# Kernel tuning notes

Hardware: AMD Instinct MI355X
Metric: run time of the kernel (lower is better)

Reference implementation:

```python
import jax, jax.numpy as jnp
import numpy as np

BLOCK = (4, 8, 8)   # (t, h, w)
NH, D, DA = 8, 512, 64
EPS = 1e-5


def _layernorm(x, g, b):
    m = jnp.mean(x, axis=-1, keepdims=True)
    xc = x - m
    v = jnp.mean(xc * xc, axis=-1, keepdims=True)
    return xc * jax.lax.rsqrt(v + EPS) * g + b


def setup_inputs() -> dict:
    key = jax.random.key(0)
    ks = jax.random.split(key, 10)
    B, T, H, W = 2, 8, 32, 32
    t, h, w = BLOCK
    s_qkv = (2.0 / (D + DA)) ** 0.5   # xavier_normal for (d, da) fan
    s_lin = (2.0 / (D + D)) ** 0.5
    return {
        "x": jax.random.normal(ks[0], (B, D, T, H, W), jnp.float32),
        "dt_bank": 0.02 * jax.random.normal(ks[1], (NH, 2 * t - 1), jnp.float32),
        "dh_bank": 0.02 * jax.random.normal(ks[2], (NH, 2 * h - 1), jnp.float32),
        "dw_bank": 0.02 * jax.random.normal(ks[3], (NH, 2 * w - 1), jnp.float32),
        "ln1_g": jnp.ones((D,), jnp.float32),
        "ln1_b": jnp.zeros((D,), jnp.float32),
        "w_q": s_qkv * jax.random.normal(ks[4], (NH, D, DA), jnp.float32),
        "w_k": s_qkv * jax.random.normal(ks[5], (NH, D, DA), jnp.float32),
        "w_v": s_qkv * jax.random.normal(ks[6], (NH, D, DA), jnp.float32),
        "w_proj": s_lin * jax.random.normal(ks[7], (D, NH * DA), jnp.float32),
        "ln2_g": jnp.ones((D,), jnp.float32),
        "ln2_b": jnp.zeros((D,), jnp.float32),
        "w1": s_lin * jax.random.normal(ks[8], (D, D), jnp.float32),
        "b1": jnp.zeros((D,), jnp.float32),
        "w2": s_lin * jax.random.normal(ks[9], (D, D), jnp.float32),
        "b2": jnp.zeros((D,), jnp.float32),
    }


def _axial_bias(dt_bank, dh_bank, dw_bank):
    t, h, w = BLOCK
    thw = t * h * w
    ar = jnp.arange(thw)
    tt = ar // (h * w)
    hh = (ar // w) % h
    ww = ar % w
    # relative offsets shifted to be non-negative (matches dt += abs(dt.min()))
    it = tt[:, None] - tt[None, :] + (t - 1)
    ih = hh[:, None] - hh[None, :] + (h - 1)
    iw = ww[:, None] - ww[None, :] + (w - 1)
    return dt_bank[:, it] + dh_bank[:, ih] + dw_bank[:, iw]  # (NH, thw, thw)


def reference(x, dt_bank, dh_bank, dw_bank, ln1_g, ln1_b, w_q, w_k, w_v,
              w_proj, ln2_g, ln2_b, w1, b1, w2, b2):
    B, C, T, H, W = x.shape
    t, h, w = BLOCK
    st, sh, sw = T // t, H // h, W // w
    thw = t * h * w
    nb = B * st * sh * sw

    # block split: (B,C,T,H,W) -> (nb, thw, C)
    xb = x.reshape(B, C, st, t, sh, h, sw, w).transpose(0, 2, 4, 6, 1, 3, 5, 7)
    xb = xb.reshape(nb, C, thw).transpose(0, 2, 1)

    Bb = _axial_bias(dt_bank, dh_bank, dw_bank)  # (NH, thw, thw)

    # --- multi-head attention with additive axial bias ---
    resid = xb
    xn = _layernorm(xb, ln1_g, ln1_b)
    q = jnp.einsum('bnd,hde->hbne', xn, w_q)
    k = jnp.einsum('bnd,hde->hbne', xn, w_k)
    v = jnp.einsum('bnd,hde->hbne', xn, w_v)
    scale = 1.0 / jnp.sqrt(jnp.asarray(DA, x.dtype))
    attn = jnp.einsum('hbne,hbme->hbnm', q, k) * scale + Bb[:, None]
    attn = jax.nn.softmax(attn, axis=-1)
    out = jnp.einsum('hbnm,hbme->hbne', attn, v)         # (NH, nb, thw, DA)
    out = out.transpose(1, 2, 0, 3).reshape(nb, thw, NH * DA)  # head-major concat
    out = out @ w_proj.T + resid

    # --- FFN with residual ---
    y = _layernorm(out, ln2_g, ln2_b)
    y = jax.nn.relu(y @ w1.T + b1) @ w2.T + b2
    out = y + out

    # un-block: (nb, thw, C) -> (B,C,T,H,W)
    out = out.transpose(0, 2, 1).reshape(B, st, sh, sw, C, t, h, w)
    out = out.transpose(0, 4, 1, 5, 2, 6, 3, 7).reshape(B, C, T, H, W)
    return out
```

## Files before the change

### kernel.cpp

```cpp
#include <hip/hip_runtime.h>
#include <hip/hip_bf16.h>
#include <stdint.h>

typedef __attribute__((ext_vector_type(4))) float f32x4;
typedef __attribute__((ext_vector_type(8))) short s16x8;
typedef __attribute__((ext_vector_type(4))) short s16x4;
typedef __attribute__((ext_vector_type(8))) __bf16 b16x8;

__device__ __forceinline__ f32x4 mfma16(s16x8 a, s16x8 b, f32x4 c) {
  return __builtin_amdgcn_mfma_f32_16x16x32_bf16(
      __builtin_bit_cast(b16x8, a), __builtin_bit_cast(b16x8, b), c, 0, 0, 0);
}

__device__ __forceinline__ void gl_lds16(const void* g, void* l) {
  __builtin_amdgcn_global_load_lds(
      (const __attribute__((address_space(1))) void*)g,
      (__attribute__((address_space(3))) void*)l, 16, 0, 0);
}

__device__ __forceinline__ unsigned short f2bf(float f) {
  union { float f; unsigned u; } v; v.f = f;
  unsigned u = v.u;
  return (unsigned short)((u + 0x7FFFu + ((u >> 16) & 1u)) >> 16);
}

__device__ __forceinline__ float bf2f(unsigned short u) {
  union { unsigned u; float f; } v; v.u = ((unsigned)u) << 16; return v.f;
}

__device__ __forceinline__ unsigned cvt_pk_bf16(float a, float b) {
  unsigned r;
  asm("v_cvt_pk_bf16_f32 %0, %1, %2" : "=v"(r) : "v"(a), "v"(b));
  return r;
}

#if __has_builtin(__builtin_amdgcn_exp2f)
#define EXP2F(x) __builtin_amdgcn_exp2f(x)
#else
#define EXP2F(x) exp2f(x)
#endif

__device__ __forceinline__ int bfrag_off(int n, int k) {
  return ((((n >> 4) * 16 + (k >> 5)) * 4 + ((k >> 3) & 3)) * 16 + (n & 15)) * 8 + (k & 7);
}

__global__ __launch_bounds__(256) void k_gather_ln(
    const float* __restrict__ x, const float* __restrict__ g1, const float* __restrict__ b1,
    unsigned short* __restrict__ xb, unsigned short* __restrict__ xn,
    const float* __restrict__ wq, const float* __restrict__ wk, const float* __restrict__ wv,
    const float* __restrict__ wp, const float* __restrict__ w1, const float* __restrict__ w2,
    unsigned short* __restrict__ qkvT, unsigned short* __restrict__ wpT,
    unsigned short* __restrict__ w1T, unsigned short* __restrict__ w2T)
{
  if (blockIdx.x >= 1024) {
    int i = (blockIdx.x - 1024) * 256 + threadIdx.x;
    if (i < 786432) {
      int n = i >> 9, d = i & 511;
      const float* src = (n < 512) ? wq : (n < 1024 ? wk : wv);
      int nn = n & 511;
      int h = nn >> 6, e = nn & 63;
      qkvT[bfrag_off(n, d)] = f2bf(src[((size_t)h * 512 + d) * 64 + e]);
    } else {
      int j = i - 786432;
      int w = j >> 18;
      int o = j & 262143;
      const float* s = (w == 0) ? wp : (w == 1 ? w1 : w2);
      unsigned short* dst = (w == 0) ? wpT : (w == 1 ? w1T : w2T);
      dst[bfrag_off(o >> 9, o & 511)] = f2bf(s[o]);
    }
    return;
  }
  __shared__ float lx[16][517];
  int gid = blockIdx.x;
  int h2 = gid & 1, hh = (gid >> 1) & 7, tt = (gid >> 4) & 3,
      shI = (gid >> 6) & 3, stI = (gid >> 8) & 1, bI = (gid >> 9) & 1;
  const float* xbase = x + (size_t)bI * 4194304 + (size_t)(stI * 4 + tt) * 1024
                       + (shI * 8 + hh) * 32 + h2 * 16;
  int t = threadIdx.x;
  for (int i = 0; i < 8; ++i) {
    int slot = i * 256 + t;
    int c = slot >> 2, w8 = slot & 3;
    const float4 v = *(const float4*)(xbase + (size_t)c * 8192 + w8 * 4);
    lx[w8 * 4 + 0][c] = v.x; lx[w8 * 4 + 1][c] = v.y;
    lx[w8 * 4 + 2][c] = v.z; lx[w8 * 4 + 3][c] = v.w;
  }
  __syncthreads();
  int lane = t & 63, wid = t >> 6;
  for (int q = 0; q < 4; ++q) {
    int widx = wid * 4 + q;
    float vv[8]; float s = 0.f, ss = 0.f;
    #pragma unroll
    for (int i = 0; i < 8; ++i) { float v = lx[widx][lane + i * 64]; vv[i] = v; s += v; ss += v * v; }
    #pragma unroll
    for (int d = 1; d < 64; d <<= 1) { s += __shfl_xor(s, d); ss += __shfl_xor(ss, d); }
    float mean = s * (1.f / 512.f);
    float var = ss * (1.f / 512.f) - mean * mean;
    float rs = rsqrtf(var + 1e-5f);
    int sw = h2 * 2 + (widx >> 3), ww = widx & 7;
    int blk = ((bI * 2 + stI) * 4 + shI) * 4 + sw;
    int n = tt * 64 + hh * 8 + ww;
    size_t base = ((size_t)blk * 256 + n) * 512;
    #pragma unroll
    for (int i = 0; i < 8; ++i) {
      int c = lane + i * 64;
      float v = vv[i];
      xb[base + c] = f2bf(v);
      xn[base + c] = f2bf((v - mean) * rs * g1[c] + b1[c]);
    }
  }
}

template<int EPI>
__global__ __launch_bounds__(256, 2) void k_gemm(
    const unsigned short* __restrict__ A, const unsigned short* __restrict__ Bt,
    int M, int N,
    unsigned short* __restrict__ Cbf, float* __restrict__ Cf,
    const float* __restrict__ bias,
    const unsigned short* __restrict__ addbf,
    unsigned short* __restrict__ vTout)
{
  constexpr int K = 512;
  __shared__ __align__(16) unsigned short a_lds[2][128 * 64];
  int tid = threadIdx.x, lane = tid & 63, wid = tid >> 6;
  int lin = blockIdx.y * gridDim.x + blockIdx.x;
  int xcd = lin & 7, idx = lin >> 3;
  int bx = xcd * 16 + (idx & 15);
  int by = idx >> 4;
  int m0 = bx * 128, n0 = by * 128;
  int wm = (wid >> 1) * 64, wn = (wid & 1) * 64;
  int r15 = lane & 15, g = lane >> 4;

  const unsigned short* aptr[4];
  int segoff[4];
  #pragma unroll
  for (int s = 0; s < 4; ++s) {
    int seg = wid * 4 + s;
    int slot = seg * 64 + lane;
    int m = slot >> 3, lc = (slot & 7) ^ (m & 7);
    aptr[s] = A + (size_t)(m0 + m) * K + lc * 8;
    segoff[s] = seg * 1024;
  }
  const unsigned short* bfbase = Bt + (size_t)((n0 + wn) >> 4) * 8192 + lane * 8;

  f32x4 acc[4][4] = {};
  s16x8 b[2][4][2];

  #pragma unroll
  for (int s = 0; s < 4; ++s) gl_lds16(aptr[s], (char*)a_lds[0] + segoff[s]);
  #pragma unroll
  for (int f = 0; f < 4; ++f)
    #pragma unroll
    for (int kk = 0; kk < 2; ++kk)
      b[0][f][kk] = *(const s16x8*)(bfbase + f * 8192 + kk * 512);

  #pragma unroll
  for (int it = 0; it < 8; ++it) {
    int cur = it & 1;
    if (it < 7) {
      int ksn = (it + 1) * 64;
      #pragma unroll
      for (int s = 0; s < 4; ++s)
        gl_lds16(aptr[s] + ksn, (char*)a_lds[cur ^ 1] + segoff[s]);
      asm volatile("s_waitcnt vmcnt(4)" ::: "memory");
    } else {
      asm volatile("s_waitcnt vmcnt(0)" ::: "memory");
    }
    __builtin_amdgcn_s_barrier();
    __builtin_amdgcn_sched_barrier(0);
    if (it < 7) {
      int kc0 = (it + 1) * 2;
      #pragma unroll
      for (int f = 0; f < 4; ++f)
        #pragma unroll
        for (int kk = 0; kk < 2; ++kk)
          b[cur ^ 1][f][kk] = *(const s16x8*)(bfbase + f * 8192 + (kc0 + kk) * 512);
    }
    const char* al = (const char*)a_lds[cur];
    #pragma unroll
    for (int kk = 0; kk < 2; ++kk) {
      s16x8 af[4];
      #pragma unroll
      for (int f = 0; f < 4; ++f) {
        int mm = wm + f * 16 + r15;
        af[f] = *(const s16x8*)(al + mm * 128 + (((kk * 4 + g) ^ (mm & 7)) * 16));
      }
      __builtin_amdgcn_s_setprio(1);
      #pragma unroll
      for (int fm = 0; fm < 4; ++fm)
        #pragma unroll
        for (int fn = 0; fn < 4; ++fn)
          acc[fm][fn] = mfma16(af[fm], b[cur][fn][kk], acc[fm][fn]);
      __builtin_amdgcn_s_setprio(0);
    }
    __builtin_amdgcn_s_barrier();
    __builtin_amdgcn_sched_barrier(0);
  }

  int g4 = g * 4;
  #pragma unroll
  for (int fm = 0; fm < 4; ++fm) {
    #pragma unroll
    for (int fn = 0; fn < 4; ++fn) {
      int col = n0 + wn + fn * 16 + r15;
      int row0 = m0 + wm + fm * 16 + g4;
      if (EPI == 0 && col >= 1024) {
        int h = (col - 1024) >> 6, e = col & 63;
        int blk = row0 >> 8, mtok = row0 & 255;
        s16x4 pk;
        #pragma unroll
        for (int r = 0; r < 4; ++r) pk[r] = (short)f2bf(acc[fm][fn][r]);
        *(s16x4*)(vTout + (((size_t)blk * 8 + h) * 64 + e) * 256 + mtok) = pk;
      } else {
        #pragma unroll
        for (int r = 0; r < 4; ++r) {
          int row = row0 + r;
          float v = acc[fm][fn][r];
          if (EPI == 0) {
            Cbf[(size_t)row * 1536 + col] = f2bf(v);
          } else if (EPI == 1) {
            Cbf[(size_t)row * 512 + col] = f2bf(v + bf2f(addbf[(size_t)row * 512 + col]));
          } else if (EPI == 2) {
            Cbf[(size_t)row * 512 + col] = f2bf(fmaxf(v + bias[col], 0.f));
          } else {
            Cf[(size_t)row * 512 + col] = v + bias[col] + bf2f(addbf[(size_t)row * 512 + col]);
          }
        }
      }
    }
  }
}

__global__ __launch_bounds__(256, 1) void k_attn(
    const unsigned short* __restrict__ qkv, const unsigned short* __restrict__ vT,
    const float* __restrict__ dtb, const float* __restrict__ dhb, const float* __restrict__ dwb,
    unsigned short* __restrict__ aout)
{
  __shared__ __align__(16) unsigned short k_lds[2][64 * 64];
  __shared__ __align__(16) unsigned short v_lds[2][64 * 64];
  __shared__ __align__(16) unsigned short p_lds[4][64 * 64];
  __shared__ float bt_s[8], bh_s[16], bw_s[16];

  const float L2E = 1.44269504f;
  const float SC = 0.125f * 1.44269504f;

  int tid = threadIdx.x, lane = tid & 63, wid = tid >> 6;
  int bk = blockIdx.x >> 3, h = blockIdx.x & 7;
  if (tid < 7) bt_s[tid] = dtb[h * 7 + tid] * L2E;
  else if (tid < 22) bh_s[tid - 7] = dhb[h * 15 + tid - 7] * L2E;
  else if (tid < 37) bw_s[tid - 22] = dwb[h * 15 + tid - 22] * L2E;

  int r15 = lane & 15, g = lane >> 4;
  int wq0 = wid * 64;
  size_t bkBase = (size_t)bk * 256;
  const unsigned short* kbase = qkv + 512 + h * 64;
  const unsigned short* vbase = vT + ((size_t)bk * 8 + h) * 64 * 256;

  s16x8 qf[4][2];
  #pragma unroll
  for (int fn = 0; fn < 4; ++fn)
    #pragma unroll
    for (int kk = 0; kk < 2; ++kk)
      qf[fn][kk] = *(const s16x8*)(qkv + (bkBase + wq0 + fn * 16 + r15) * 1536
                                   + h * 64 + kk * 32 + g * 8);

  float btoff[4], hb[7], wb[4];

  #pragma unroll
  for (int s = 0; s < 4; ++s) {
    int sg = wid * 4 + s;
    if (sg < 8) {
      int slot = sg * 64 + lane;
      int m = slot >> 3, lc = (slot & 7) ^ (m & 7);
      gl_lds16(kbase + (bkBase + m) * 1536 + lc * 8, (char*)(&k_lds[0][0]) + sg * 1024);
    } else {
      int sg2 = sg - 8;
      int slot = sg2 * 64 + lane;
      int e = slot >> 3, lc = (slot & 7) ^ (e & 7);
      gl_lds16(vbase + (size_t)e * 256 + lc * 8, (char*)(&v_lds[0][0]) + sg2 * 1024);
    }
  }
  __syncthreads();

  {
    int Dh = (r15 >> 3) - (g >> 1) + 7;
    int Wb = (r15 & 7) - 4 * (g & 1) + 7;
    #pragma unroll
    for (int mt = 0; mt < 4; ++mt) btoff[mt] = bt_s[wid + 3 - mt];
    #pragma unroll
    for (int d = 0; d < 7; ++d) hb[d] = bh_s[Dh + 2 * d - 6];
    #pragma unroll
    for (int r = 0; r < 4; ++r) wb[r] = bw_s[Wb - r];
  }

  f32x4 o[4][4] = {};
  float mrun[4] = {-1e30f, -1e30f, -1e30f, -1e30f};
  float lrun[4] = {0.f, 0.f, 0.f, 0.f};
  char* p_w = (char*)(&p_lds[wid][0]);

  #pragma unroll
  for (int mt = 0; mt < 4; ++mt) {
    int cur = mt & 1;
    if (mt < 3) {
      int m0n = (mt + 1) * 64;
      #pragma unroll
      for (int s = 0; s < 4; ++s) {
        int sg = wid * 4 + s;
        if (sg < 8) {
          int slot = sg * 64 + lane;
          int m = slot >> 3, lc = (slot & 7) ^ (m & 7);
          gl_lds16(kbase + (bkBase + m0n + m) * 1536 + lc * 8,
                   (char*)(&k_lds[cur ^ 1][0]) + sg * 1024);
        } else {
          int sg2 = sg - 8;
          int slot = sg2 * 64 + lane;
          int e = slot >> 3, lc = (slot & 7) ^ (e & 7);
          gl_lds16(vbase + (size_t)e * 256 + m0n + lc * 8,
                   (char*)(&v_lds[cur ^ 1][0]) + sg2 * 1024);
        }
      }
    }
    if (mt > 0) {
      if (mt < 3) asm volatile("s_waitcnt vmcnt(4)" ::: "memory");
      else        asm volatile("s_waitcnt vmcnt(0)" ::: "memory");
      __builtin_amdgcn_s_barrier();
      __builtin_amdgcn_sched_barrier(0);
    }
    const char* kl = (const char*)(&k_lds[cur][0]);
    const char* vl = (const char*)(&v_lds[cur][0]);

    f32x4 st[4][4] = {};
    #pragma unroll
    for (int kk = 0; kk < 2; ++kk) {
      s16x8 kf[4];
      #pragma unroll
      for (int fm = 0; fm < 4; ++fm) {
        int m = fm * 16 + r15;
        kf[fm] = *(const s16x8*)(kl + m * 128 + (((kk * 4 + g) ^ (m & 7)) * 16));
      }
      __builtin_amdgcn_s_setprio(1);
      #pragma unroll
      for (int fm = 0; fm < 4; ++fm)
        #pragma unroll
        for (int fn = 0; fn < 4; ++fn)
          st[fm][fn] = mfma16(kf[fm], qf[fn][kk], st[fm][fn]);
      __builtin_amdgcn_s_setprio(0);
    }

    #pragma unroll
    for (int fn = 0; fn < 4; ++fn) {
      float vals[16];
      float mx = -1e30f;
      #pragma unroll
      for (int fm = 0; fm < 4; ++fm) {
        float cc = btoff[mt] + hb[fn - fm + 3];
        #pragma unroll
        for (int r = 0; r < 4; ++r) {
          float v = fmaf(st[fm][fn][r], SC, cc) + wb[r];
          vals[fm * 4 + r] = v;
          mx = fmaxf(mx, v);
        }
      }
      mx = fmaxf(mx, __shfl_xor(mx, 16));
      mx = fmaxf(mx, __shfl_xor(mx, 32));
      if (!__all(mx <= mrun[fn] + 8.f)) {
        float mnew = fmaxf(mrun[fn], mx);
        float al = EXP2F(mrun[fn] - mnew);
        mrun[fn] = mnew;
        lrun[fn] *= al;
        #pragma unroll
        for (int fe = 0; fe < 4; ++fe)
          #pragma unroll
          for (int r = 0; r < 4; ++r)
            o[fe][fn][r] *= al;
      }
      float m_c = mrun[fn];
      float p[16]; float sum = 0.f;
      #pragma unroll
      for (int i = 0; i < 16; ++i) { p[i] = EXP2F(vals[i] - m_c); sum += p[i]; }
      sum += __shfl_xor(sum, 16);
      sum += __shfl_xor(sum, 32);
      lrun[fn] += sum;
      int nl = fn * 16 + r15;
      char* prow = p_w + nl * 128 + (g & 1) * 8;
      #pragma unroll
      for (int fm = 0; fm < 4; ++fm) {
        unsigned u0 = cvt_pk_bf16(p[fm * 4 + 0], p[fm * 4 + 1]);
        unsigned u1 = cvt_pk_bf16(p[fm * 4 + 2], p[fm * 4 + 3]);
        int lc = fm * 2 + (g >> 1);
        *(uint2*)(prow + ((lc ^ (nl & 7)) * 16)) = make_uint2(u0, u1);
      }
    }
    asm volatile("s_waitcnt lgkmcnt(0)" ::: "memory");
    __builtin_amdgcn_sched_barrier(0);

    #pragma unroll
    for (int mm = 0; mm < 2; ++mm) {
      s16x8 vf[4], pf[4];
      #pragma unroll
      for (int fe = 0; fe < 4; ++fe) {
        int e = fe * 16 + r15;
        vf[fe] = *(const s16x8*)(vl + e * 128 + (((mm * 4 + g) ^ (e & 7)) * 16));
      }
      #pragma unroll
      for (int fn = 0; fn < 4; ++fn) {
        int nl = fn * 16 + r15;
        pf[fn] = *(const s16x8*)(p_w + nl * 128 + (((mm * 4 + g) ^ (nl & 7)) * 16));
      }
      __builtin_amdgcn_s_setprio(1);
      #pragma unroll
      for (int fe = 0; fe < 4; ++fe)
        #pragma unroll
        for (int fn = 0; fn < 4; ++fn)
          o[fe][fn] = mfma16(vf[fe], pf[fn], o[fe][fn]);
      __builtin_amdgcn_s_setprio(0);
    }
    __builtin_amdgcn_s_barrier();
    __builtin_amdgcn_sched_barrier(0);
  }

  #pragma unroll
  for (int fn = 0; fn < 4; ++fn) {
    float inv = 1.f / lrun[fn];
    size_t rowb = (bkBase + wq0 + fn * 16 + r15) * 512 + h * 64;
    #pragma unroll
    for (int fe = 0; fe < 4; ++fe) {
      unsigned u0 = cvt_pk_bf16(o[fe][fn][0] * inv, o[fe][fn][1] * inv);
      unsigned u1 = cvt_pk_bf16(o[fe][fn][2] * inv, o[fe][fn][3] * inv);
      *(uint2*)(aout + rowb + fe * 16 + g * 4) = make_uint2(u0, u1);
    }
  }
}

__global__ __launch_bounds__(256) void k_ln2(
    const unsigned short* __restrict__ in, const float* __restrict__ g2, const float* __restrict__ b2,
    unsigned short* __restrict__ out)
{
  int token = blockIdx.x * 4 + (threadIdx.x >> 6);
  int lane = threadIdx.x & 63;
  s16x8 v8 = *(const s16x8*)(in + (size_t)token * 512 + lane * 8);
  float vv[8]; float s = 0.f, ss = 0.f;
  #pragma unroll
  for (int i = 0; i < 8; ++i) {
    float v = bf2f((unsigned short)v8[i]); vv[i] = v; s += v; ss += v * v;
  }
  #pragma unroll
  for (int d = 1; d < 64; d <<= 1) { s += __shfl_xor(s, d); ss += __shfl_xor(ss, d); }
  float mean = s * (1.f / 512.f);
  float var = ss * (1.f / 512.f) - mean * mean;
  float rs = rsqrtf(var + 1e-5f);
  const float4 gA = *(const float4*)(g2 + lane * 8);
  const float4 gB = *(const float4*)(g2 + lane * 8 + 4);
  const float4 bA = *(const float4*)(b2 + lane * 8);
  const float4 bB = *(const float4*)(b2 + lane * 8 + 4);
  float gv[8] = {gA.x, gA.y, gA.z, gA.w, gB.x, gB.y, gB.z, gB.w};
  float bv[8] = {bA.x, bA.y, bA.z, bA.w, bB.x, bB.y, bB.z, bB.w};
  s16x8 o8;
  #pragma unroll
  for (int i = 0; i < 8; ++i)
    o8[i] = (short)f2bf((vv[i] - mean) * rs * gv[i] + bv[i]);
  *(s16x8*)(out + (size_t)token * 512 + lane * 8) = o8;
}

__global__ __launch_bounds__(64) void k_scatter(
    const float* __restrict__ fin, float* __restrict__ out)
{
  __shared__ float lx[32][33];
  int gid = blockIdx.x;
  int cc = gid & 15;
  int sg = gid >> 4;
  int hh = sg & 7, tt = (sg >> 3) & 3, shI = (sg >> 5) & 3, stI = (sg >> 7) & 1, bI = (sg >> 8) & 1;
  int c0 = cc * 32;
  int l = threadIdx.x;
  #pragma unroll
  for (int i = 0; i < 4; ++i) {
    int slot = i * 64 + l;
    int tok = slot >> 3, c4 = slot & 7;
    int blk = ((bI * 2 + stI) * 4 + shI) * 4 + (tok >> 3);
    int n = tt * 64 + hh * 8 + (tok & 7);
    const float4 v = *(const float4*)(fin + ((size_t)blk * 256 + n) * 512 + c0 + c4 * 4);
    lx[tok][c4 * 4 + 0] = v.x; lx[tok][c4 * 4 + 1] = v.y;
    lx[tok][c4 * 4 + 2] = v.z; lx[tok][c4 * 4 + 3] = v.w;
  }
  __syncthreads();
  size_t obase = (size_t)bI * 4194304 + (size_t)(stI * 4 + tt) * 1024 + (shI * 8 + hh) * 32;
  #pragma unroll
  for (int i = 0; i < 4; ++i) {
    int crow = i * 8 + (l >> 3), w4 = l & 7;
    float4 v;
    v.x = lx[w4 * 4 + 0][crow]; v.y = lx[w4 * 4 + 1][crow];
    v.z = lx[w4 * 4 + 2][crow]; v.w = lx[w4 * 4 + 3][crow];
    *(float4*)(out + obase + (size_t)(c0 + crow) * 8192 + w4 * 4) = v;
  }
}

extern "C" void kernel_launch(void* const* d_in, const int* in_sizes, int n_in,
                              void* d_out, int out_size, void* d_ws, size_t ws_size,
                              hipStream_t stream)
{
  const float* x   = (const float*)d_in[0];
  const float* dtb = (const float*)d_in[1];
  const float* dhb = (const float*)d_in[2];
  const float* dwb = (const float*)d_in[3];
  const float* g1  = (const float*)d_in[4];
  const float* bb1 = (const float*)d_in[5];
  const float* wq  = (const float*)d_in[6];
  const float* wk  = (const float*)d_in[7];
  const float* wv  = (const float*)d_in[8];
  const float* wp  = (const float*)d_in[9];
  const float* g2  = (const float*)d_in[10];
  const float* bb2 = (const float*)d_in[11];
  const float* w1  = (const float*)d_in[12];
  const float* fb1 = (const float*)d_in[13];
  const float* w2  = (const float*)d_in[14];
  const float* fb2 = (const float*)d_in[15];

  char* ws = (char*)d_ws;
  unsigned short* xb   = (unsigned short*)(ws + 0);
  float*          finalb = (float*)(ws + 0);
  unsigned short* vT   = (unsigned short*)(ws + 33554432);
  unsigned short* out1b= (unsigned short*)(ws + 33554432);
  unsigned short* qkv  = (unsigned short*)(ws + 67108864);
  unsigned short* xn   = (unsigned short*)(ws + 117440512);
  unsigned short* qkvT = (unsigned short*)(ws + 134217728);
  unsigned short* wpT  = (unsigned short*)(ws + 135790592);
  unsigned short* w1T  = (unsigned short*)(ws + 136314880);
  unsigned short* w2T  = (unsigned short*)(ws + 136839168);

  unsigned short* attn_out = xn;
  unsigned short* yb = xn;
  unsigned short* h1 = qkv;
  float* outp = (float*)d_out;

  k_gather_ln<<<1024 + 6144, 256, 0, stream>>>(x, g1, bb1, xb, xn,
      wq, wk, wv, wp, w1, w2, qkvT, wpT, w1T, w2T);
  k_gemm<0><<<dim3(128, 12), 256, 0, stream>>>(xn, qkvT, 16384, 1536, qkv, nullptr, nullptr, nullptr, vT);
  k_attn<<<512, 256, 0, stream>>>(qkv, vT, dtb, dhb, dwb, attn_out);
  k_gemm<1><<<dim3(128, 4), 256, 0, stream>>>(attn_out, wpT, 16384, 512, out1b, nullptr, nullptr, xb, nullptr);
  k_ln2<<<4096, 256, 0, stream>>>(out1b, g2, bb2, yb);
  k_gemm<2><<<dim3(128, 4), 256, 0, stream>>>(yb, w1T, 16384, 512, h1, nullptr, fb1, nullptr, nullptr);
  k_gemm<3><<<dim3(128, 4), 256, 0, stream>>>(h1, w2T, 16384, 512, nullptr, finalb, fb2, out1b, nullptr);
  k_scatter<<<8192, 64, 0, stream>>>(finalb, outp);
}
```

Baseline: 159.3 us.

## Enlarge GEMM tiles to 256x128 with 8 waves and vectorize the epilogue

The GEMM kernels now use 512-thread blocks computing 256x128 output tiles. The A tile in LDS doubles and the grid is halved along M, so each B fragment load is reused across more rows. The MFMA operand order is swapped so each lane's accumulator holds four consecutive columns of one row. That lets the epilogue issue packed bf16 and float4 stores and vector loads for bias and residual instead of scalar ones. The tighter launch bounds, 512 threads with a minimum of 4 blocks, may force register caps that cause spilling. The larger LDS footprint also reduces how many blocks fit per CU.

```diff
diff --git a/kernel.cpp b/kernel.cpp
--- a/kernel.cpp
+++ b/kernel.cpp
@@ -111,7 +111,7 @@
 }
 
 template<int EPI>
-__global__ __launch_bounds__(256, 2) void k_gemm(
+__global__ __launch_bounds__(512, 4) void k_gemm(
     const unsigned short* __restrict__ A, const unsigned short* __restrict__ Bt,
     int M, int N,
     unsigned short* __restrict__ Cbf, float* __restrict__ Cf,
@@ -120,13 +120,13 @@
     unsigned short* __restrict__ vTout)
 {
   constexpr int K = 512;
-  __shared__ __align__(16) unsigned short a_lds[2][128 * 64];
+  __shared__ __align__(16) unsigned short a_lds[2][256 * 64];
   int tid = threadIdx.x, lane = tid & 63, wid = tid >> 6;
   int lin = blockIdx.y * gridDim.x + blockIdx.x;
   int xcd = lin & 7, idx = lin >> 3;
-  int bx = xcd * 16 + (idx & 15);
-  int by = idx >> 4;
-  int m0 = bx * 128, n0 = by * 128;
+  int bx = xcd * 8 + (idx & 7);
+  int by = idx >> 3;
+  int m0 = bx * 256, n0 = by * 128;
   int wm = (wid >> 1) * 64, wn = (wid & 1) * 64;
   int r15 = lane & 15, g = lane >> 4;
 
@@ -189,42 +189,50 @@
       for (int fm = 0; fm < 4; ++fm)
         #pragma unroll
         for (int fn = 0; fn < 4; ++fn)
-          acc[fm][fn] = mfma16(af[fm], b[cur][fn][kk], acc[fm][fn]);
+          acc[fm][fn] = mfma16(b[cur][fn][kk], af[fm], acc[fm][fn]);
       __builtin_amdgcn_s_setprio(0);
     }
     __builtin_amdgcn_s_barrier();
     __builtin_amdgcn_sched_barrier(0);
   }
 
-  int g4 = g * 4;
   #pragma unroll
   for (int fm = 0; fm < 4; ++fm) {
+    int m = m0 + wm + fm * 16 + r15;
     #pragma unroll
     for (int fn = 0; fn < 4; ++fn) {
-      int col = n0 + wn + fn * 16 + r15;
-      int row0 = m0 + wm + fm * 16 + g4;
-      if (EPI == 0 && col >= 1024) {
-        int h = (col - 1024) >> 6, e = col & 63;
-        int blk = row0 >> 8, mtok = row0 & 255;
-        s16x4 pk;
-        #pragma unroll
-        for (int r = 0; r < 4; ++r) pk[r] = (short)f2bf(acc[fm][fn][r]);
-        *(s16x4*)(vTout + (((size_t)blk * 8 + h) * 64 + e) * 256 + mtok) = pk;
+      int nc = n0 + wn + fn * 16 + g * 4;
+      f32x4 v = acc[fm][fn];
+      if (EPI == 0 && nc >= 1024) {
+        int h = (nc - 1024) >> 6, e0 = nc & 63;
+        int blk = m >> 8, tok = m & 255;
+        size_t vb = (((size_t)blk * 8 + h) * 64 + e0) * 256 + tok;
+        #pragma unroll
+        for (int r = 0; r < 4; ++r) vTout[vb + (size_t)r * 256] = f2bf(v[r]);
+      } else if (EPI == 0) {
+        *(uint2*)(Cbf + (size_t)m * 1536 + nc) =
+            make_uint2(cvt_pk_bf16(v[0], v[1]), cvt_pk_bf16(v[2], v[3]));
+      } else if (EPI == 1) {
+        s16x4 a4 = *(const s16x4*)(addbf + (size_t)m * 512 + nc);
+        #pragma unroll
+        for (int r = 0; r < 4; ++r) v[r] += bf2f((unsigned short)a4[r]);
+        *(uint2*)(Cbf + (size_t)m * 512 + nc) =
+            make_uint2(cvt_pk_bf16(v[0], v[1]), cvt_pk_bf16(v[2], v[3]));
+      } else if (EPI == 2) {
+        const float4 b4 = *(const float4*)(bias + nc);
+        v[0] = fmaxf(v[0] + b4.x, 0.f); v[1] = fmaxf(v[1] + b4.y, 0.f);
+        v[2] = fmaxf(v[2] + b4.z, 0.f); v[3] = fmaxf(v[3] + b4.w, 0.f);
+        *(uint2*)(Cbf + (size_t)m * 512 + nc) =
+            make_uint2(cvt_pk_bf16(v[0], v[1]), cvt_pk_bf16(v[2], v[3]));
       } else {
-        #pragma unroll
-        for (int r = 0; r < 4; ++r) {
-          int row = row0 + r;
-          float v = acc[fm][fn][r];
-          if (EPI == 0) {
-            Cbf[(size_t)row * 1536 + col] = f2bf(v);
-          } else if (EPI == 1) {
-            Cbf[(size_t)row * 512 + col] = f2bf(v + bf2f(addbf[(size_t)row * 512 + col]));
-          } else if (EPI == 2) {
-            Cbf[(size_t)row * 512 + col] = f2bf(fmaxf(v + bias[col], 0.f));
-          } else {
-            Cf[(size_t)row * 512 + col] = v + bias[col] + bf2f(addbf[(size_t)row * 512 + col]);
-          }
-        }
+        const float4 b4 = *(const float4*)(bias + nc);
+        s16x4 a4 = *(const s16x4*)(addbf + (size_t)m * 512 + nc);
+        float4 o;
+        o.x = v[0] + b4.x + bf2f((unsigned short)a4[0]);
+        o.y = v[1] + b4.y + bf2f((unsigned short)a4[1]);
+        o.z = v[2] + b4.z + bf2f((unsigned short)a4[2]);
+        o.w = v[3] + b4.w + bf2f((unsigned short)a4[3]);
+        *(float4*)(Cf + (size_t)m * 512 + nc) = o;
       }
     }
   }
@@ -533,11 +541,11 @@
 
   k_gather_ln<<<1024 + 6144, 256, 0, stream>>>(x, g1, bb1, xb, xn,
       wq, wk, wv, wp, w1, w2, qkvT, wpT, w1T, w2T);
-  k_gemm<0><<<dim3(128, 12), 256, 0, stream>>>(xn, qkvT, 16384, 1536, qkv, nullptr, nullptr, nullptr, vT);
+  k_gemm<0><<<dim3(64, 12), 512, 0, stream>>>(xn, qkvT, 16384, 1536, qkv, nullptr, nullptr, nullptr, vT);
   k_attn<<<512, 256, 0, stream>>>(qkv, vT, dtb, dhb, dwb, attn_out);
-  k_gemm<1><<<dim3(128, 4), 256, 0, stream>>>(attn_out, wpT, 16384, 512, out1b, nullptr, nullptr, xb, nullptr);
+  k_gemm<1><<<dim3(64, 4), 512, 0, stream>>>(attn_out, wpT, 16384, 512, out1b, nullptr, nullptr, xb, nullptr);
   k_ln2<<<4096, 256, 0, stream>>>(out1b, g2, bb2, yb);
-  k_gemm<2><<<dim3(128, 4), 256, 0, stream>>>(yb, w1T, 16384, 512, h1, nullptr, fb1, nullptr, nullptr);
-  k_gemm<3><<<dim3(128, 4), 256, 0, stream>>>(h1, w2T, 16384, 512, nullptr, finalb, fb2, out1b, nullptr);
+  k_gemm<2><<<dim3(64, 4), 512, 0, stream>>>(yb, w1T, 16384, 512, h1, nullptr, fb1, nullptr, nullptr);
+  k_gemm<3><<<dim3(64, 4), 512, 0, stream>>>(h1, w2T, 16384, 512, nullptr, finalb, fb2, out1b, nullptr);
   k_scatter<<<8192, 64, 0, stream>>>(finalb, outp);
 }
```

Result: slower. 355.9 us (+123.5%).
